# Kernel tuning notes

Measured on AMD Instinct MI355X. Metric: run time of the kernel, lower is better.

Reference implementation:

```python
import jax, jax.numpy as jnp
import numpy as np

B, I, H = 32768, 128, 128


def setup_inputs() -> dict:
    key = jax.random.key(0)
    ks = jax.random.split(key, 11)
    s = 1.0 / np.sqrt(H)
    return {
        "x": jax.random.normal(ks[0], (B, I), jnp.float32),
        "h": jax.random.normal(ks[1], (B, H), jnp.float32),
        "c": jax.random.normal(ks[2], (B, H), jnp.float32),
        "W1": jax.random.normal(ks[3], (H, I + H), jnp.float32) * s,
        "b1": jax.random.normal(ks[4], (H,), jnp.float32) * s + 1.0,  # forget-gate bias offset 1.0
        "W2": jax.random.normal(ks[5], (H, I + H), jnp.float32) * s,
        "b2": jax.random.normal(ks[6], (H,), jnp.float32) * s,
        "Wf": jax.random.normal(ks[7], (H, I + H), jnp.float32) * s,
        "bf": jax.random.normal(ks[8], (H,), jnp.float32) * s,
        "W3": jax.random.normal(ks[9], (H, I + H), jnp.float32) * s,
        "b3": jax.random.normal(ks[10], (H,), jnp.float32) * s,
    }


def reference(x, h, c, W1, b1, W2, b2, Wf, bf, W3, b3):
    # total_in = inp + hidden (coordinate-list concat == feature concat)
    total = jnp.concatenate([x, h], axis=-1)  # [B, I+H]
    sig1 = jax.nn.sigmoid(total @ W1.T + b1)  # forget gate (bias offset +1)
    sig2 = jax.nn.sigmoid(total @ W2.T + b2)  # input gate
    f_l = jnp.tanh(total @ Wf.T + bf)         # candidate via symmetric f
    sig3 = jax.nn.sigmoid(total @ W3.T + b3)  # output gate
    new_c = c * sig1 + sig2 * f_l             # fused elementwise combine
    new_h = jnp.tanh(new_c) * sig3
    return new_h, new_c
```

## Files before the change

kernel.cpp:

```cpp
#include <hip/hip_runtime.h>

#define B_TOTAL 32768
#define NROWB   128
#define TILE    32
#define NT      4

typedef __attribute__((ext_vector_type(8)))  short    bf16x8;
typedef __attribute__((ext_vector_type(4)))  float    f32x4;
typedef __attribute__((ext_vector_type(4)))  unsigned u32x4;

__device__ __forceinline__ unsigned rne1(float f) {
    unsigned u = __builtin_bit_cast(unsigned, f);
    return (u + 0x7FFFu + ((u >> 16) & 1u)) >> 16;
}
__device__ __forceinline__ unsigned cvtpk(float lo, float hi) {
    unsigned r;
    asm("v_cvt_pk_bf16_f32 %0, %1, %2" : "=v"(r) : "v"(lo), "v"(hi));
    return r;
}
__device__ __forceinline__ float fsig(float v) {
    return __fdividef(1.0f, 1.0f + __expf(-v));
}
__device__ __forceinline__ float ftanh(float v) {
    return 1.0f - __fdividef(2.0f, 1.0f + __expf(2.0f * v));
}

__global__ void wconv_kernel(const float* __restrict__ w1, const float* __restrict__ w2,
                             const float* __restrict__ wf, const float* __restrict__ w3,
                             u32x4* __restrict__ out) {
    int T = blockIdx.x * 256 + threadIdx.x;
    int F = T >> 6, l = T & 63;
    int cs = F >> 5, g = (F >> 3) & 3, ks = F & 7;
    const float* W = (g == 0) ? w1 : (g == 1) ? w2 : (g == 2) ? wf : w3;
    const float* s = W + (cs * 16 + (l & 15)) * 256 + ks * 32 + (l >> 4) * 8;
    f32x4 lo = *(const f32x4*)s;
    f32x4 hi = *(const f32x4*)(s + 4);
    u32x4 r;
    r[0] = rne1(lo[0]) | (rne1(lo[1]) << 16);
    r[1] = rne1(lo[2]) | (rne1(lo[3]) << 16);
    r[2] = rne1(hi[0]) | (rne1(hi[1]) << 16);
    r[3] = rne1(hi[2]) | (rne1(hi[3]) << 16);
    out[T] = r;
}

__global__ __launch_bounds__(512, 2) void lstm_kernel(
    const float* __restrict__ x, const float* __restrict__ h, const float* __restrict__ c,
    const bf16x8* __restrict__ wfrag,
    const float* __restrict__ b1, const float* __restrict__ b2,
    const float* __restrict__ bfv, const float* __restrict__ b3,
    float* __restrict__ out)
{
    __shared__ __align__(16) char smem[2][16384];

    const int tid  = threadIdx.x;
    const int wave = tid >> 6;
    const int lane = tid & 63;
    const int rb   = lane & 15;
    const int c4   = lane >> 4;
    const long row0 = (long)blockIdx.x * NROWB;
    const int gcol4 = wave * 16 + c4 * 4;

    const int srow   = wave * 4 + (lane >> 4);
    const int kchunk = lane & 15;

    f32x4 ar[4];
    auto A_ISSUE = [&](int t) {
        const float* base = (kchunk < 8)
            ? (x + (row0 + (long)t * TILE + srow) * 128 + kchunk * 16)
            : (h + (row0 + (long)t * TILE + srow) * 128 + (kchunk - 8) * 16);
        ar[0] = *(const f32x4*)(base);
        ar[1] = *(const f32x4*)(base + 4);
        ar[2] = *(const f32x4*)(base + 8);
        ar[3] = *(const f32x4*)(base + 12);
    };
    auto A_STORE = [&](int b) {
        u32x4 w0, w1;
        w0[0] = cvtpk(ar[0][0], ar[0][1]);
        w0[1] = cvtpk(ar[0][2], ar[0][3]);
        w0[2] = cvtpk(ar[1][0], ar[1][1]);
        w0[3] = cvtpk(ar[1][2], ar[1][3]);
        w1[0] = cvtpk(ar[2][0], ar[2][1]);
        w1[1] = cvtpk(ar[2][2], ar[2][3]);
        w1[2] = cvtpk(ar[3][0], ar[3][1]);
        w1[3] = cvtpk(ar[3][2], ar[3][3]);
        char* dst = smem[b & 1] + (kchunk >> 1) * 2048 + srow * 64 + (kchunk & 1) * 32;
        *(u32x4*)(dst)      = w0;
        *(u32x4*)(dst + 16) = w1;
    };

    A_ISSUE(0);

    bf16x8 wfr[4][8];
#pragma unroll
    for (int g = 0; g < 4; ++g)
#pragma unroll
        for (int ks = 0; ks < 8; ++ks)
            wfr[g][ks] = wfrag[(size_t)(wave * 32 + g * 8 + ks) * 64 + lane];

    f32x4 bias[4];
    bias[0] = *(const f32x4*)(b1 + gcol4);
    bias[1] = *(const f32x4*)(b2 + gcol4);
    bias[2] = *(const f32x4*)(bfv + gcol4);
    bias[3] = *(const f32x4*)(b3 + gcol4);

    A_STORE(0);
    A_ISSUE(1);

    f32x4 cv0 = *(const f32x4*)(c + (row0 + rb) * 128 + gcol4);
    f32x4 cv1 = *(const f32x4*)(c + (row0 + 16 + rb) * 128 + gcol4);

    float* out_h = out;
    float* out_c = out + (size_t)B_TOTAL * 128;

#pragma unroll 1
    for (int t = 0; t < NT; ++t) {
        asm volatile("s_waitcnt lgkmcnt(0)" ::: "memory");
        __builtin_amdgcn_s_barrier();
        __builtin_amdgcn_sched_barrier(0);

        const char* buf = smem[t & 1];
        const long gr0 = row0 + (long)t * TILE;

        f32x4 acc[2][4];
#pragma unroll
        for (int g = 0; g < 4; ++g) { acc[0][g] = bias[g]; acc[1][g] = bias[g]; }

#pragma unroll
        for (int ks = 0; ks < 8; ++ks) {
            bf16x8 af0 = *(const bf16x8*)(buf + ks * 2048 + rb * 64 + c4 * 16);
            bf16x8 af1 = *(const bf16x8*)(buf + ks * 2048 + (16 + rb) * 64 + c4 * 16);
#pragma unroll
            for (int g = 0; g < 4; ++g) {
                acc[0][g] = __builtin_amdgcn_mfma_f32_16x16x32_bf16(wfr[g][ks], af0, acc[0][g], 0, 0, 0);
                acc[1][g] = __builtin_amdgcn_mfma_f32_16x16x32_bf16(wfr[g][ks], af1, acc[1][g], 0, 0, 0);
            }
        }

        if (t + 1 < NT) {
            A_STORE(t + 1);
            if (t + 2 < NT) A_ISSUE(t + 2);
        }

        f32x4 ncv0, ncv1;
        if (t + 1 < NT) {
            ncv0 = *(const f32x4*)(c + (gr0 + TILE + rb) * 128 + gcol4);
            ncv1 = *(const f32x4*)(c + (gr0 + TILE + 16 + rb) * 128 + gcol4);
        }

#pragma unroll
        for (int mt = 0; mt < 2; ++mt) {
            const f32x4 cv = mt ? cv1 : cv0;
            f32x4 nh, nc;
#pragma unroll
            for (int j = 0; j < 4; ++j) {
                const float g1 = fsig(acc[mt][0][j]);
                const float g2 = fsig(acc[mt][1][j]);
                const float gf = ftanh(acc[mt][2][j]);
                const float g3 = fsig(acc[mt][3][j]);
                nc[j] = cv[j] * g1 + g2 * gf;
                nh[j] = ftanh(nc[j]) * g3;
            }
            const long o = (gr0 + mt * 16 + rb) * 128 + gcol4;
            *(f32x4*)(out_h + o) = nh;
            *(f32x4*)(out_c + o) = nc;
        }

        if (t + 1 < NT) { cv0 = ncv0; cv1 = ncv1; }
    }
}

extern "C" void kernel_launch(void* const* d_in, const int* in_sizes, int n_in,
                              void* d_out, int out_size, void* d_ws, size_t ws_size,
                              hipStream_t stream) {
    (void)in_sizes; (void)n_in; (void)out_size; (void)ws_size;
    const float* x  = (const float*)d_in[0];
    const float* h  = (const float*)d_in[1];
    const float* c  = (const float*)d_in[2];
    const float* W1 = (const float*)d_in[3];
    const float* b1 = (const float*)d_in[4];
    const float* W2 = (const float*)d_in[5];
    const float* b2 = (const float*)d_in[6];
    const float* Wf = (const float*)d_in[7];
    const float* bf = (const float*)d_in[8];
    const float* W3 = (const float*)d_in[9];
    const float* b3 = (const float*)d_in[10];

    wconv_kernel<<<64, 256, 0, stream>>>(W1, W2, Wf, W3, (u32x4*)d_ws);
    lstm_kernel<<<B_TOTAL / NROWB, 512, 0, stream>>>(
        x, h, c, (const bf16x8*)d_ws, b1, b2, bf, b3, (float*)d_out);
}
```

Baseline: 32.41 us.

## Defer LSTM epilogue by one tile to overlap with next tile's MFMAs

The tile loop is fully unrolled and the accumulators are kept per tile, so the sigmoid/tanh epilogue and stores for tile t-1 run after tile t's MFMA chain is issued. The transcendental VALU work can then overlap with the in-flight matrix ops instead of waiting on them. The cost is a larger live accumulator set per thread, which raises register pressure under launch_bounds(512,2) and risks spills.

```diff
diff --git a/kernel.cpp b/kernel.cpp
--- a/kernel.cpp
+++ b/kernel.cpp
@@ -106,24 +106,45 @@
     A_STORE(0);
     A_ISSUE(1);
 
-    f32x4 cv0 = *(const f32x4*)(c + (row0 + rb) * 128 + gcol4);
-    f32x4 cv1 = *(const f32x4*)(c + (row0 + 16 + rb) * 128 + gcol4);
-
     float* out_h = out;
     float* out_c = out + (size_t)B_TOTAL * 128;
 
-#pragma unroll 1
+    f32x4 acc[NT][2][4];
+    f32x4 cv[NT][2];
+
+    cv[0][0] = *(const f32x4*)(c + (row0 + rb) * 128 + gcol4);
+    cv[0][1] = *(const f32x4*)(c + (row0 + 16 + rb) * 128 + gcol4);
+
+    auto EPI = [&](int tt) {
+        const long gr0 = row0 + (long)tt * TILE;
+#pragma unroll
+        for (int mt = 0; mt < 2; ++mt) {
+            f32x4 nh, nc;
+#pragma unroll
+            for (int j = 0; j < 4; ++j) {
+                const float g1 = fsig(acc[tt][mt][0][j]);
+                const float g2 = fsig(acc[tt][mt][1][j]);
+                const float gf = ftanh(acc[tt][mt][2][j]);
+                const float g3 = fsig(acc[tt][mt][3][j]);
+                nc[j] = cv[tt][mt][j] * g1 + g2 * gf;
+                nh[j] = ftanh(nc[j]) * g3;
+            }
+            const long o = (gr0 + mt * 16 + rb) * 128 + gcol4;
+            *(f32x4*)(out_h + o) = nh;
+            *(f32x4*)(out_c + o) = nc;
+        }
+    };
+
+#pragma unroll
     for (int t = 0; t < NT; ++t) {
         asm volatile("s_waitcnt lgkmcnt(0)" ::: "memory");
         __builtin_amdgcn_s_barrier();
         __builtin_amdgcn_sched_barrier(0);
 
         const char* buf = smem[t & 1];
-        const long gr0 = row0 + (long)t * TILE;
 
-        f32x4 acc[2][4];
 #pragma unroll
-        for (int g = 0; g < 4; ++g) { acc[0][g] = bias[g]; acc[1][g] = bias[g]; }
+        for (int g = 0; g < 4; ++g) { acc[t][0][g] = bias[g]; acc[t][1][g] = bias[g]; }
 
 #pragma unroll
         for (int ks = 0; ks < 8; ++ks) {
@@ -131,8 +152,8 @@
             bf16x8 af1 = *(const bf16x8*)(buf + ks * 2048 + (16 + rb) * 64 + c4 * 16);
 #pragma unroll
             for (int g = 0; g < 4; ++g) {
-                acc[0][g] = __builtin_amdgcn_mfma_f32_16x16x32_bf16(wfr[g][ks], af0, acc[0][g], 0, 0, 0);
-                acc[1][g] = __builtin_amdgcn_mfma_f32_16x16x32_bf16(wfr[g][ks], af1, acc[1][g], 0, 0, 0);
+                acc[t][0][g] = __builtin_amdgcn_mfma_f32_16x16x32_bf16(wfr[g][ks], af0, acc[t][0][g], 0, 0, 0);
+                acc[t][1][g] = __builtin_amdgcn_mfma_f32_16x16x32_bf16(wfr[g][ks], af1, acc[t][1][g], 0, 0, 0);
             }
         }
 
@@ -141,32 +162,16 @@
             if (t + 2 < NT) A_ISSUE(t + 2);
         }
 
-        f32x4 ncv0, ncv1;
+        if (t > 0) EPI(t - 1);
+
         if (t + 1 < NT) {
-            ncv0 = *(const f32x4*)(c + (gr0 + TILE + rb) * 128 + gcol4);
-            ncv1 = *(const f32x4*)(c + (gr0 + TILE + 16 + rb) * 128 + gcol4);
+            const long nr0 = row0 + (long)(t + 1) * TILE;
+            cv[t + 1][0] = *(const f32x4*)(c + (nr0 + rb) * 128 + gcol4);
+            cv[t + 1][1] = *(const f32x4*)(c + (nr0 + 16 + rb) * 128 + gcol4);
         }
+    }
 
-#pragma unroll
-        for (int mt = 0; mt < 2; ++mt) {
-            const f32x4 cv = mt ? cv1 : cv0;
-            f32x4 nh, nc;
-#pragma unroll
-            for (int j = 0; j < 4; ++j) {
-                const float g1 = fsig(acc[mt][0][j]);
-                const float g2 = fsig(acc[mt][1][j]);
-                const float gf = ftanh(acc[mt][2][j]);
-                const float g3 = fsig(acc[mt][3][j]);
-                nc[j] = cv[j] * g1 + g2 * gf;
-                nh[j] = ftanh(nc[j]) * g3;
-            }
-            const long o = (gr0 + mt * 16 + rb) * 128 + gcol4;
-            *(f32x4*)(out_h + o) = nh;
-            *(f32x4*)(out_c + o) = nc;
-        }
-
-        if (t + 1 < NT) { cv0 = ncv0; cv1 = ncv1; }
-    }
+    EPI(NT - 1);
 }
 
 extern "C" void kernel_launch(void* const* d_in, const int* in_sizes, int n_in,
```

Measured after the change: 55.42 us. 71.0% more time.
